# Kernel tuning notes

Hardware: AMD Instinct MI355X
Metric: run time of the kernel (lower is better)

Reference implementation:

```python
import jax, jax.numpy as jnp
import numpy as np

SIZE = 4096  # core_size(16) ** nr_cores(3)


def setup_inputs() -> dict:
    key = jax.random.key(0)
    k_x, k0, k1, k2, kb = jax.random.split(key, 5)
    d, r = 16, 64
    # std per TT.init_core: sigma = (t * sqrt(r)**(1-c))**(1/c), t=1/sqrt(size), c=3
    t = 1.0 / np.sqrt(SIZE)
    sigma = float((t * np.sqrt(r) ** (1 - 3)) ** (1.0 / 3))
    x = jax.random.normal(k_x, (4, 2048, SIZE), dtype=jnp.float32)
    g0 = sigma * jax.random.normal(k0, (1, d, d, r), dtype=jnp.float32)
    g1 = sigma * jax.random.normal(k1, (r, d, d, r), dtype=jnp.float32)
    g2 = sigma * jax.random.normal(k2, (r, d, d, 1), dtype=jnp.float32)
    bias = np.sqrt(1.0 / SIZE) * jax.random.uniform(kb, (SIZE,), dtype=jnp.float32, minval=-1.0, maxval=1.0)
    return {"x": x, "g0": g0, "g1": g1, "g2": g2, "bias": bias}


def reference(x, g0, g1, g2, bias):
    # to_matrix: chain of einsum contractions over TT cores
    G = g0[0]  # (d, d, r)
    G = jnp.einsum('ija,aklb->ijklb', G, g1)      # (d,d,d,d,r)
    G = jnp.einsum('ijkla,amnb->ijklmnb', G, g2)  # (d,d,d,d,d,d,1)
    G = G.reshape(SIZE, SIZE)
    # forward: flatten leading dims, dense matmul + bias, restore shape
    X = x.reshape(-1, SIZE)
    out = X @ G + bias
    return out.reshape(*x.shape[:-1], SIZE)
```

## Files before the change

kernel.cpp:

```cpp
#include <hip/hip_runtime.h>
#include <stdint.h>

#define DI __device__ __forceinline__

using floatx4 = __attribute__((ext_vector_type(4))) float;
using short8  = __attribute__((ext_vector_type(8))) short;

DI uint16_t f2b(float f) {
  uint32_t u = __float_as_uint(f);
  return (uint16_t)((u + 0x7FFFu + ((u >> 16) & 1u)) >> 16);
}

DI void async_cp16(const uint16_t* g, uint16_t* l) {
  __builtin_amdgcn_global_load_lds(
      (const __attribute__((address_space(1))) void*)g,
      (__attribute__((address_space(3))) void*)l, 16, 0, 0);
}

__global__ __launch_bounds__(256)
void cvt_bf16(const float* __restrict__ x, uint16_t* __restrict__ y) {
  long i = ((long)blockIdx.x * 256 + threadIdx.x) * 8;
  float4 a = *(const float4*)(x + i);
  float4 b = *(const float4*)(x + i + 4);
  union { uint16_t u[8]; uint4 v; } o;
  o.u[0] = f2b(a.x); o.u[1] = f2b(a.y); o.u[2] = f2b(a.z); o.u[3] = f2b(a.w);
  o.u[4] = f2b(b.x); o.u[5] = f2b(b.y); o.u[6] = f2b(b.z); o.u[7] = f2b(b.w);
  *(uint4*)(y + i) = o.v;
}

__global__ __launch_bounds__(256)
void tt_t1(const float* __restrict__ g0, const float* __restrict__ g1,
           uint16_t* __restrict__ t1) {
  __shared__ float g0s[64 * 64];
  __shared__ float g1s[64 * 128];
  const int rowbase = blockIdx.x * 64;
  const int colbase = blockIdx.y * 128;
  const int t = threadIdx.x;

  for (int f = t; f < 4096; f += 256) g0s[f] = g0[rowbase * 64 + f];
  for (int f = t; f < 8192; f += 256) {
    int a = f >> 7, c = f & 127;
    g1s[f] = g1[(long)a * 16384 + colbase + c];
  }
  __syncthreads();

  const int tx = t & 31;
  const int ty = t >> 5;
  const int c0 = tx * 4;
  const int r0 = ty * 8;

  float acc[8][4];
  #pragma unroll
  for (int r = 0; r < 8; ++r)
    #pragma unroll
    for (int c = 0; c < 4; ++c) acc[r][c] = 0.f;

  for (int a4 = 0; a4 < 16; ++a4) {
    float g0r[8][4];
    #pragma unroll
    for (int r = 0; r < 8; ++r)
      *(float4*)&g0r[r][0] = *(const float4*)&g0s[(r0 + r) * 64 + a4 * 4];
    #pragma unroll
    for (int e = 0; e < 4; ++e) {
      float4 bv4 = *(const float4*)&g1s[(a4 * 4 + e) * 128 + c0];
      float bv[4] = {bv4.x, bv4.y, bv4.z, bv4.w};
      #pragma unroll
      for (int r = 0; r < 8; ++r)
        #pragma unroll
        for (int c = 0; c < 4; ++c)
          acc[r][c] += g0r[r][e] * bv[c];
    }
  }

  #pragma unroll
  for (int r = 0; r < 8; ++r) {
    ushort4 o;
    o.x = f2b(acc[r][0]); o.y = f2b(acc[r][1]);
    o.z = f2b(acc[r][2]); o.w = f2b(acc[r][3]);
    *(ushort4*)&t1[(long)(rowbase + r0 + r) * 16384 + colbase + c0] = o;
  }
}

__global__ __launch_bounds__(256)
void transpose_t1(const uint16_t* __restrict__ src, uint16_t* __restrict__ dst,
                  const float* __restrict__ g2, uint16_t* __restrict__ g2t) {
  __shared__ uint16_t tile[64][68];
  const int cb = blockIdx.x * 64;
  const int rb = blockIdx.y * 64;
  const int t = threadIdx.x;

  if (blockIdx.y == 0) {
    #pragma unroll
    for (int p = 0; p < 4; ++p) {
      int f = blockIdx.x * 1024 + p * 256 + t;
      int mn = f >> 6, b = f & 63;
      g2t[f] = f2b(g2[b * 256 + mn]);
    }
  }
  {
    const int c4 = (t & 15) * 4;
    const int r  = t >> 4;
    #pragma unroll
    for (int p = 0; p < 4; ++p) {
      int rr = r + p * 16;
      *(ushort4*)&tile[rr][c4] = *(const ushort4*)&src[(long)(rb + rr) * 1024 + cb + c4];
    }
  }
  __syncthreads();
  {
    const int r4 = (t & 15) * 4;
    const int c  = t >> 4;
    #pragma unroll
    for (int p = 0; p < 4; ++p) {
      int cc = c + p * 16;
      ushort4 o;
      o.x = tile[r4 + 0][cc]; o.y = tile[r4 + 1][cc];
      o.z = tile[r4 + 2][cc]; o.w = tile[r4 + 3][cc];
      *(ushort4*)&dst[(long)(cb + cc) * 4096 + rb + r4] = o;
    }
  }
}

#define VSTRIDE 136

DI void compute_half(const uint16_t* __restrict__ as_, const uint16_t* __restrict__ bs_,
                     int wm, int wn, int fr, int fk, floatx4 acc[4][4]) {
  short8 af[4], bg[4];
  #pragma unroll
  for (int i = 0; i < 4; ++i)
    af[i] = *(const short8*)&as_[(wm + i * 16 + fr) * 32 + fk];
  #pragma unroll
  for (int j = 0; j < 4; ++j)
    bg[j] = *(const short8*)&bs_[(wn + j * 16 + fr) * 32 + fk];
  #pragma unroll
  for (int i = 0; i < 4; ++i)
    #pragma unroll
    for (int j = 0; j < 4; ++j)
      acc[i][j] = __builtin_amdgcn_mfma_f32_16x16x32_bf16(af[i], bg[j], acc[i][j], 0, 0, 0);
}

DI void stage_tile(const uint16_t* __restrict__ Ab, const uint16_t* __restrict__ Bb,
                   uint16_t* dstbuf, int k0, int wave, int srow, int scol) {
  #pragma unroll
  for (int ks = 0; ks < 2; ++ks)
    #pragma unroll
    for (int t = 0; t < 2; ++t) {
      const int rblk = wave * 2 + t;
      async_cp16(Ab + (long)(rblk * 16 + srow) * 4096 + k0 + ks * 32 + scol,
                 dstbuf + ks * 4096 + rblk * 16 * 32);
      async_cp16(Bb + (long)(rblk * 16 + srow) * 4096 + k0 + ks * 32 + scol,
                 dstbuf + 8192 + ks * 4096 + rblk * 16 * 32);
    }
}

__global__ __launch_bounds__(256, 2)
void gemm_fused(const uint16_t* __restrict__ A,
                const uint16_t* __restrict__ Bt,
                const uint16_t* __restrict__ g2t,
                const float* __restrict__ bias,
                float* __restrict__ out) {
  __shared__ __align__(16) uint16_t lds[32768];
  uint16_t* buf0 = lds;
  uint16_t* buf1 = lds + 16384;

  const int bm = blockIdx.x * 128;
  const int bn = blockIdx.y * 128;
  const int tid  = threadIdx.x;
  const int wave = tid >> 6;
  const int lane = tid & 63;
  const int wm = (wave >> 1) * 64;
  const int wn = (wave & 1) * 64;

  const uint16_t* Ab = A + (long)bm * 4096;
  const uint16_t* Bb = Bt + (long)bn * 4096;

  const int srow = lane >> 2;
  const int scol = (lane & 3) * 8;
  const int fr = lane & 15;
  const int fk = (lane >> 4) * 8;

  floatx4 acc[4][4];
  #pragma unroll
  for (int i = 0; i < 4; ++i)
    #pragma unroll
    for (int j = 0; j < 4; ++j)
      acc[i][j] = (floatx4){0.f, 0.f, 0.f, 0.f};

  stage_tile(Ab, Bb, buf0, 0, wave, srow, scol);
  __syncthreads();

  for (int t = 0; t < 62; t += 2) {
    stage_tile(Ab, Bb, buf1, (t + 1) * 64, wave, srow, scol);
    compute_half(buf0,        buf0 + 8192,  wm, wn, fr, fk, acc);
    compute_half(buf0 + 4096, buf0 + 12288, wm, wn, fr, fk, acc);
    __syncthreads();

    stage_tile(Ab, Bb, buf0, (t + 2) * 64, wave, srow, scol);
    compute_half(buf1,        buf1 + 8192,  wm, wn, fr, fk, acc);
    compute_half(buf1 + 4096, buf1 + 12288, wm, wn, fr, fk, acc);
    __syncthreads();
  }
  stage_tile(Ab, Bb, buf1, 63 * 64, wave, srow, scol);
  compute_half(buf0,        buf0 + 8192,  wm, wn, fr, fk, acc);
  compute_half(buf0 + 4096, buf0 + 12288, wm, wn, fr, fk, acc);
  __syncthreads();
  compute_half(buf1,        buf1 + 8192,  wm, wn, fr, fk, acc);
  compute_half(buf1 + 4096, buf1 + 12288, wm, wn, fr, fk, acc);

  const int colq = lane & 15;
  const int rowq = (lane >> 4) * 4;
  __syncthreads();
  #pragma unroll
  for (int i = 0; i < 4; ++i)
    #pragma unroll
    for (int j = 0; j < 4; ++j)
      #pragma unroll
      for (int r = 0; r < 4; ++r)
        lds[(wm + i * 16 + rowq + r) * VSTRIDE + wn + j * 16 + colq] = f2b(acc[i][j][r]);
  __syncthreads();

  const int bsel   = (wave >> 1) * 64;
  const int mnBase = (wave & 1) * 128;
  const long ocol0 = (long)blockIdx.y * 512 + (wave >> 1) * 256 + mnBase;

  short8 bg2[8][2];
  #pragma unroll
  for (int jn = 0; jn < 8; ++jn)
    #pragma unroll
    for (int ks = 0; ks < 2; ++ks)
      bg2[jn][ks] = *(const short8*)&g2t[(mnBase + jn * 16 + fr) * 64 + ks * 32 + fk];

  float bvs[8];
  #pragma unroll
  for (int jn = 0; jn < 8; ++jn)
    bvs[jn] = bias[ocol0 + jn * 16 + colq];

  #pragma unroll
  for (int pass = 0; pass < 4; ++pass) {
    floatx4 acc2[2][8];
    #pragma unroll
    for (int im = 0; im < 2; ++im)
      #pragma unroll
      for (int jn = 0; jn < 8; ++jn)
        acc2[im][jn] = (floatx4){0.f, 0.f, 0.f, 0.f};

    short8 af2[2][2];
    #pragma unroll
    for (int im = 0; im < 2; ++im)
      #pragma unroll
      for (int ks = 0; ks < 2; ++ks)
        af2[im][ks] = *(const short8*)&lds[(pass * 32 + im * 16 + fr) * VSTRIDE + bsel + ks * 32 + fk];

    #pragma unroll
    for (int im = 0; im < 2; ++im)
      #pragma unroll
      for (int jn = 0; jn < 8; ++jn)
        #pragma unroll
        for (int ks = 0; ks < 2; ++ks)
          acc2[im][jn] = __builtin_amdgcn_mfma_f32_16x16x32_bf16(af2[im][ks], bg2[jn][ks], acc2[im][jn], 0, 0, 0);

    #pragma unroll
    for (int jn = 0; jn < 8; ++jn)
      #pragma unroll
      for (int im = 0; im < 2; ++im)
        #pragma unroll
        for (int r = 0; r < 4; ++r) {
          const int row = bm + pass * 32 + im * 16 + rowq + r;
          out[(long)row * 4096 + ocol0 + jn * 16 + colq] = acc2[im][jn][r] + bvs[jn];
        }
  }
}

static constexpr long XBF_OFF = 0;
static constexpr long T1_OFF  = 67108864;
static constexpr long T1T_OFF = 75497472;
static constexpr long G2T_OFF = 83886080;

extern "C" void kernel_launch(void* const* d_in, const int* in_sizes, int n_in,
                              void* d_out, int out_size, void* d_ws, size_t ws_size,
                              hipStream_t stream) {
  const float* x    = (const float*)d_in[0];
  const float* g0   = (const float*)d_in[1];
  const float* g1   = (const float*)d_in[2];
  const float* g2   = (const float*)d_in[3];
  const float* bias = (const float*)d_in[4];
  float* out = (float*)d_out;

  char* ws = (char*)d_ws;
  uint16_t* Xbf = (uint16_t*)(ws + XBF_OFF);
  uint16_t* T1  = (uint16_t*)(ws + T1_OFF);
  uint16_t* T1t = (uint16_t*)(ws + T1T_OFF);
  uint16_t* G2T = (uint16_t*)(ws + G2T_OFF);

  cvt_bf16<<<16384, 256, 0, stream>>>(x, Xbf);
  tt_t1<<<dim3(4, 128), 256, 0, stream>>>(g0, g1, T1);
  transpose_t1<<<dim3(16, 64), 256, 0, stream>>>(T1, T1t, g2, G2T);
  gemm_fused<<<dim3(64, 8), 256, 0, stream>>>(Xbf, T1t, G2T, bias, out);
}
```

Measured before the change: 335.0 us.

## Merge prep kernels, write T1 transposed directly, use 32x32 MFMA with swizzled LDS

Folds the bf16 conversion, the TT core contraction and the g2 transpose into one prep launch, writing T1 straight into its transposed layout so the separate transpose kernel and its intermediate buffer go away. The main GEMM moves from 16x16x32 to 32x32x16 bf16 MFMA and XOR-swizzles the LDS chunk placement to cut bank conflicts on fragment loads. The directly transposed T1 writes are scattered 2-byte stores, which may cost more than the transpose they replace. The prep launch also uses fewer, longer-running blocks for the x conversion.

```diff
diff --git a/kernel.cpp b/kernel.cpp
--- a/kernel.cpp
+++ b/kernel.cpp
@@ -3,8 +3,9 @@
 
 #define DI __device__ __forceinline__
 
-using floatx4 = __attribute__((ext_vector_type(4))) float;
-using short8  = __attribute__((ext_vector_type(8))) short;
+using floatx4  = __attribute__((ext_vector_type(4)))  float;
+using floatx16 = __attribute__((ext_vector_type(16))) float;
+using short8   = __attribute__((ext_vector_type(8)))  short;
 
 DI uint16_t f2b(float f) {
   uint32_t u = __float_as_uint(f);
@@ -18,139 +19,126 @@
 }
 
 __global__ __launch_bounds__(256)
-void cvt_bf16(const float* __restrict__ x, uint16_t* __restrict__ y) {
-  long i = ((long)blockIdx.x * 256 + threadIdx.x) * 8;
-  float4 a = *(const float4*)(x + i);
-  float4 b = *(const float4*)(x + i + 4);
-  union { uint16_t u[8]; uint4 v; } o;
-  o.u[0] = f2b(a.x); o.u[1] = f2b(a.y); o.u[2] = f2b(a.z); o.u[3] = f2b(a.w);
-  o.u[4] = f2b(b.x); o.u[5] = f2b(b.y); o.u[6] = f2b(b.z); o.u[7] = f2b(b.w);
-  *(uint4*)(y + i) = o.v;
-}
-
-__global__ __launch_bounds__(256)
-void tt_t1(const float* __restrict__ g0, const float* __restrict__ g1,
-           uint16_t* __restrict__ t1) {
-  __shared__ float g0s[64 * 64];
-  __shared__ float g1s[64 * 128];
-  const int rowbase = blockIdx.x * 64;
-  const int colbase = blockIdx.y * 128;
+void prep(const float* __restrict__ x, uint16_t* __restrict__ Xbf,
+          const float* __restrict__ g0, const float* __restrict__ g1,
+          uint16_t* __restrict__ t1t,
+          const float* __restrict__ g2, uint16_t* __restrict__ g2t) {
+  const int bid = blockIdx.x;
   const int t = threadIdx.x;
 
-  for (int f = t; f < 4096; f += 256) g0s[f] = g0[rowbase * 64 + f];
-  for (int f = t; f < 8192; f += 256) {
-    int a = f >> 7, c = f & 127;
-    g1s[f] = g1[(long)a * 16384 + colbase + c];
-  }
-  __syncthreads();
-
-  const int tx = t & 31;
-  const int ty = t >> 5;
-  const int c0 = tx * 4;
-  const int r0 = ty * 8;
-
-  float acc[8][4];
-  #pragma unroll
-  for (int r = 0; r < 8; ++r)
-    #pragma unroll
-    for (int c = 0; c < 4; ++c) acc[r][c] = 0.f;
-
-  for (int a4 = 0; a4 < 16; ++a4) {
-    float g0r[8][4];
+  if (bid < 512) {
+    __shared__ float g0s[64 * 64];
+    __shared__ float g1s[64 * 128];
+    const int bx = bid >> 7;
+    const int by = bid & 127;
+    const int rowbase = bx * 64;
+    const int colbase = by * 128;
+
+    if (bid < 16) {
+      #pragma unroll
+      for (int p = 0; p < 4; ++p) {
+        int f = bid * 1024 + p * 256 + t;
+        int mn = f >> 6, b = f & 63;
+        g2t[f] = f2b(g2[b * 256 + mn]);
+      }
+    }
+    for (int f = t; f < 4096; f += 256) g0s[f] = g0[rowbase * 64 + f];
+    for (int f = t; f < 8192; f += 256) {
+      int a = f >> 7, c = f & 127;
+      g1s[f] = g1[(long)a * 16384 + colbase + c];
+    }
+    __syncthreads();
+
+    const int tx = t & 31;
+    const int ty = t >> 5;
+    const int c0 = tx * 4;
+    const int r0 = ty * 8;
+
+    float acc[8][4];
     #pragma unroll
     for (int r = 0; r < 8; ++r)
-      *(float4*)&g0r[r][0] = *(const float4*)&g0s[(r0 + r) * 64 + a4 * 4];
-    #pragma unroll
-    for (int e = 0; e < 4; ++e) {
-      float4 bv4 = *(const float4*)&g1s[(a4 * 4 + e) * 128 + c0];
-      float bv[4] = {bv4.x, bv4.y, bv4.z, bv4.w};
+      #pragma unroll
+      for (int c = 0; c < 4; ++c) acc[r][c] = 0.f;
+
+    for (int a4 = 0; a4 < 16; ++a4) {
+      float g0r[8][4];
       #pragma unroll
       for (int r = 0; r < 8; ++r)
-        #pragma unroll
-        for (int c = 0; c < 4; ++c)
-          acc[r][c] += g0r[r][e] * bv[c];
-    }
-  }
-
-  #pragma unroll
-  for (int r = 0; r < 8; ++r) {
-    ushort4 o;
-    o.x = f2b(acc[r][0]); o.y = f2b(acc[r][1]);
-    o.z = f2b(acc[r][2]); o.w = f2b(acc[r][3]);
-    *(ushort4*)&t1[(long)(rowbase + r0 + r) * 16384 + colbase + c0] = o;
-  }
-}
-
-__global__ __launch_bounds__(256)
-void transpose_t1(const uint16_t* __restrict__ src, uint16_t* __restrict__ dst,
-                  const float* __restrict__ g2, uint16_t* __restrict__ g2t) {
-  __shared__ uint16_t tile[64][68];
-  const int cb = blockIdx.x * 64;
-  const int rb = blockIdx.y * 64;
-  const int t = threadIdx.x;
-
-  if (blockIdx.y == 0) {
-    #pragma unroll
-    for (int p = 0; p < 4; ++p) {
-      int f = blockIdx.x * 1024 + p * 256 + t;
-      int mn = f >> 6, b = f & 63;
-      g2t[f] = f2b(g2[b * 256 + mn]);
-    }
-  }
-  {
-    const int c4 = (t & 15) * 4;
-    const int r  = t >> 4;
-    #pragma unroll
-    for (int p = 0; p < 4; ++p) {
-      int rr = r + p * 16;
-      *(ushort4*)&tile[rr][c4] = *(const ushort4*)&src[(long)(rb + rr) * 1024 + cb + c4];
-    }
-  }
-  __syncthreads();
-  {
-    const int r4 = (t & 15) * 4;
-    const int c  = t >> 4;
-    #pragma unroll
-    for (int p = 0; p < 4; ++p) {
-      int cc = c + p * 16;
-      ushort4 o;
-      o.x = tile[r4 + 0][cc]; o.y = tile[r4 + 1][cc];
-      o.z = tile[r4 + 2][cc]; o.w = tile[r4 + 3][cc];
-      *(ushort4*)&dst[(long)(cb + cc) * 4096 + rb + r4] = o;
+        *(float4*)&g0r[r][0] = *(const float4*)&g0s[(r0 + r) * 64 + a4 * 4];
+      #pragma unroll
+      for (int e = 0; e < 4; ++e) {
+        float4 bv4 = *(const float4*)&g1s[(a4 * 4 + e) * 128 + c0];
+        float bv[4] = {bv4.x, bv4.y, bv4.z, bv4.w};
+        #pragma unroll
+        for (int r = 0; r < 8; ++r)
+          #pragma unroll
+          for (int c = 0; c < 4; ++c)
+            acc[r][c] += g0r[r][e] * bv[c];
+      }
+    }
+
+    const int k   = colbase >> 10;
+    const int lb0 = (colbase & 1023) + c0;
+    #pragma unroll
+    for (int r = 0; r < 8; ++r)
+      #pragma unroll
+      for (int c = 0; c < 4; ++c)
+        t1t[(long)(lb0 + c) * 4096 + (rowbase + r0 + r) * 16 + k] = f2b(acc[r][c]);
+  } else {
+    const int cb = bid - 512;
+    for (int pass = 0; pass < 8; ++pass) {
+      long i = (((long)pass * 2048 + cb) * 256 + t) * 8;
+      float4 a = *(const float4*)(x + i);
+      float4 b = *(const float4*)(x + i + 4);
+      union { uint16_t u[8]; uint4 v; } o;
+      o.u[0] = f2b(a.x); o.u[1] = f2b(a.y); o.u[2] = f2b(a.z); o.u[3] = f2b(a.w);
+      o.u[4] = f2b(b.x); o.u[5] = f2b(b.y); o.u[6] = f2b(b.z); o.u[7] = f2b(b.w);
+      *(uint4*)(Xbf + i) = o.v;
     }
   }
 }
 
 #define VSTRIDE 136
 
-DI void compute_half(const uint16_t* __restrict__ as_, const uint16_t* __restrict__ bs_,
-                     int wm, int wn, int fr, int fk, floatx4 acc[4][4]) {
-  short8 af[4], bg[4];
-  #pragma unroll
-  for (int i = 0; i < 4; ++i)
-    af[i] = *(const short8*)&as_[(wm + i * 16 + fr) * 32 + fk];
-  #pragma unroll
-  for (int j = 0; j < 4; ++j)
-    bg[j] = *(const short8*)&bs_[(wn + j * 16 + fr) * 32 + fk];
-  #pragma unroll
-  for (int i = 0; i < 4; ++i)
-    #pragma unroll
-    for (int j = 0; j < 4; ++j)
-      acc[i][j] = __builtin_amdgcn_mfma_f32_16x16x32_bf16(af[i], bg[j], acc[i][j], 0, 0, 0);
+DI short8 ld_swz(const uint16_t* half, int row, int c) {
+  return *(const short8*)&half[row * 32 + ((c ^ ((row >> 1) & 3)) << 3)];
 }
 
 DI void stage_tile(const uint16_t* __restrict__ Ab, const uint16_t* __restrict__ Bb,
-                   uint16_t* dstbuf, int k0, int wave, int srow, int scol) {
+                   uint16_t* dstbuf, int k0, int wave, int srow, int schunk8) {
   #pragma unroll
   for (int ks = 0; ks < 2; ++ks)
     #pragma unroll
     for (int t = 0; t < 2; ++t) {
       const int rblk = wave * 2 + t;
-      async_cp16(Ab + (long)(rblk * 16 + srow) * 4096 + k0 + ks * 32 + scol,
+      async_cp16(Ab + (long)(rblk * 16 + srow) * 4096 + k0 + ks * 32 + schunk8,
                  dstbuf + ks * 4096 + rblk * 16 * 32);
-      async_cp16(Bb + (long)(rblk * 16 + srow) * 4096 + k0 + ks * 32 + scol,
+      async_cp16(Bb + (long)(rblk * 16 + srow) * 4096 + k0 + ks * 32 + schunk8,
                  dstbuf + 8192 + ks * 4096 + rblk * 16 * 32);
     }
+}
+
+DI void compute_half32(const uint16_t* __restrict__ as_, const uint16_t* __restrict__ bs_,
+                       int wm, int wn, int lane, floatx16 acc[2][2]) {
+  const int r32 = lane & 31;
+  const int ch  = lane >> 5;
+  short8 af[2][2], bg[2][2];
+  #pragma unroll
+  for (int s = 0; s < 2; ++s) {
+    #pragma unroll
+    for (int i = 0; i < 2; ++i)
+      af[i][s] = ld_swz(as_, wm + i * 32 + r32, s * 2 + ch);
+    #pragma unroll
+    for (int j = 0; j < 2; ++j)
+      bg[j][s] = ld_swz(bs_, wn + j * 32 + r32, s * 2 + ch);
+  }
+  #pragma unroll
+  for (int s = 0; s < 2; ++s)
+    #pragma unroll
+    for (int i = 0; i < 2; ++i)
+      #pragma unroll
+      for (int j = 0; j < 2; ++j)
+        acc[i][j] = __builtin_amdgcn_mfma_f32_32x32x16_bf16(af[i][s], bg[j][s], acc[i][j], 0, 0, 0);
 }
 
 __global__ __launch_bounds__(256, 2)
@@ -164,7 +152,6 @@
   uint16_t* buf1 = lds + 16384;
 
   const int bm = blockIdx.x * 128;
-  const int bn = blockIdx.y * 128;
   const int tid  = threadIdx.x;
   const int wave = tid >> 6;
   const int lane = tid & 63;
@@ -172,53 +159,60 @@
   const int wn = (wave & 1) * 64;
 
   const uint16_t* Ab = A + (long)bm * 4096;
-  const uint16_t* Bb = Bt + (long)bn * 4096;
-
-  const int srow = lane >> 2;
-  const int scol = (lane & 3) * 8;
+  const uint16_t* Bb = Bt + (long)blockIdx.y * 128 * 4096;
+
+  const int srow    = lane >> 2;
+  const int schunk8 = (((lane & 3) ^ ((lane >> 3) & 3)) << 3);
+
+  floatx16 acc[2][2];
+  #pragma unroll
+  for (int i = 0; i < 2; ++i)
+    #pragma unroll
+    for (int j = 0; j < 2; ++j)
+      #pragma unroll
+      for (int r = 0; r < 16; ++r) acc[i][j][r] = 0.f;
+
+  stage_tile(Ab, Bb, buf0, 0, wave, srow, schunk8);
+  __syncthreads();
+
+  for (int t = 0; t < 62; t += 2) {
+    stage_tile(Ab, Bb, buf1, (t + 1) * 64, wave, srow, schunk8);
+    compute_half32(buf0,        buf0 + 8192,  wm, wn, lane, acc);
+    compute_half32(buf0 + 4096, buf0 + 12288, wm, wn, lane, acc);
+    __syncthreads();
+
+    stage_tile(Ab, Bb, buf0, (t + 2) * 64, wave, srow, schunk8);
+    compute_half32(buf1,        buf1 + 8192,  wm, wn, lane, acc);
+    compute_half32(buf1 + 4096, buf1 + 12288, wm, wn, lane, acc);
+    __syncthreads();
+  }
+  stage_tile(Ab, Bb, buf1, 63 * 64, wave, srow, schunk8);
+  compute_half32(buf0,        buf0 + 8192,  wm, wn, lane, acc);
+  compute_half32(buf0 + 4096, buf0 + 12288, wm, wn, lane, acc);
+  __syncthreads();
+  compute_half32(buf1,        buf1 + 8192,  wm, wn, lane, acc);
+  compute_half32(buf1 + 4096, buf1 + 12288, wm, wn, lane, acc);
+
+  __syncthreads();
+  {
+    const int cc = lane & 31;
+    const int rh = (lane >> 5) * 4;
+    #pragma unroll
+    for (int i = 0; i < 2; ++i)
+      #pragma unroll
+      for (int j = 0; j < 2; ++j)
+        #pragma unroll
+        for (int r = 0; r < 16; ++r) {
+          const int rr = (r & 3) + 8 * (r >> 2) + rh;
+          lds[(wm + i * 32 + rr) * VSTRIDE + wn + j * 32 + cc] = f2b(acc[i][j][r]);
+        }
+  }
+  __syncthreads();
+
   const int fr = lane & 15;
   const int fk = (lane >> 4) * 8;
-
-  floatx4 acc[4][4];
-  #pragma unroll
-  for (int i = 0; i < 4; ++i)
-    #pragma unroll
-    for (int j = 0; j < 4; ++j)
-      acc[i][j] = (floatx4){0.f, 0.f, 0.f, 0.f};
-
-  stage_tile(Ab, Bb, buf0, 0, wave, srow, scol);
-  __syncthreads();
-
-  for (int t = 0; t < 62; t += 2) {
-    stage_tile(Ab, Bb, buf1, (t + 1) * 64, wave, srow, scol);
-    compute_half(buf0,        buf0 + 8192,  wm, wn, fr, fk, acc);
-    compute_half(buf0 + 4096, buf0 + 12288, wm, wn, fr, fk, acc);
-    __syncthreads();
-
-    stage_tile(Ab, Bb, buf0, (t + 2) * 64, wave, srow, scol);
-    compute_half(buf1,        buf1 + 8192,  wm, wn, fr, fk, acc);
-    compute_half(buf1 + 4096, buf1 + 12288, wm, wn, fr, fk, acc);
-    __syncthreads();
-  }
-  stage_tile(Ab, Bb, buf1, 63 * 64, wave, srow, scol);
-  compute_half(buf0,        buf0 + 8192,  wm, wn, fr, fk, acc);
-  compute_half(buf0 + 4096, buf0 + 12288, wm, wn, fr, fk, acc);
-  __syncthreads();
-  compute_half(buf1,        buf1 + 8192,  wm, wn, fr, fk, acc);
-  compute_half(buf1 + 4096, buf1 + 12288, wm, wn, fr, fk, acc);
-
   const int colq = lane & 15;
   const int rowq = (lane >> 4) * 4;
-  __syncthreads();
-  #pragma unroll
-  for (int i = 0; i < 4; ++i)
-    #pragma unroll
-    for (int j = 0; j < 4; ++j)
-      #pragma unroll
-      for (int r = 0; r < 4; ++r)
-        lds[(wm + i * 16 + rowq + r) * VSTRIDE + wn + j * 16 + colq] = f2b(acc[i][j][r]);
-  __syncthreads();
-
   const int bsel   = (wave >> 1) * 64;
   const int mnBase = (wave & 1) * 128;
   const long ocol0 = (long)blockIdx.y * 512 + (wave >> 1) * 256 + mnBase;
@@ -272,9 +266,8 @@
 }
 
 static constexpr long XBF_OFF = 0;
-static constexpr long T1_OFF  = 67108864;
-static constexpr long T1T_OFF = 75497472;
-static constexpr long G2T_OFF = 83886080;
+static constexpr long T1T_OFF = 67108864;
+static constexpr long G2T_OFF = 75497472;
 
 extern "C" void kernel_launch(void* const* d_in, const int* in_sizes, int n_in,
                               void* d_out, int out_size, void* d_ws, size_t ws_size,
@@ -288,12 +281,9 @@
 
   char* ws = (char*)d_ws;
   uint16_t* Xbf = (uint16_t*)(ws + XBF_OFF);
-  uint16_t* T1  = (uint16_t*)(ws + T1_OFF);
   uint16_t* T1t = (uint16_t*)(ws + T1T_OFF);
   uint16_t* G2T = (uint16_t*)(ws + G2T_OFF);
 
-  cvt_bf16<<<16384, 256, 0, stream>>>(x, Xbf);
-  tt_t1<<<dim3(4, 128), 256, 0, stream>>>(g0, g1, T1);
-  transpose_t1<<<dim3(16, 64), 256, 0, stream>>>(T1, T1t, g2, G2T);
+  prep<<<2560, 256, 0, stream>>>(x, Xbf, g0, g1, T1t, g2, G2T);
   gemm_fused<<<dim3(64, 8), 256, 0, stream>>>(Xbf, T1t, G2T, bias, out);
 }
```

After: 374.6 us. 1.12x slower.
